# Kernel optimization log

Measured on AMD Instinct MI355X. Metric: run time of the kernel, lower is better.

## Reference

```python
import jax, jax.numpy as jnp
import numpy as np
import math

NUM_BINS = 10
TAIL_BOUND = 5.0
FILTER_CHANNELS = 192
KERNEL_SIZE = 3
N_LAYERS = 3
HALF = 1
MIN_BIN = 1e-3
MIN_DERIV = 1e-3


def conv1d(x, w, b, dilation=1, groups=1, padding=0):
    # x: [B,C,T], w: [O, C//groups, K]
    y = jax.lax.conv_general_dilated(
        x, w, window_strides=(1,), padding=[(padding, padding)],
        rhs_dilation=(dilation,), dimension_numbers=('NCH', 'OIH', 'NCH'),
        feature_group_count=groups)
    return y + b[None, :, None]


def ln_channels(x, g, b, eps=1e-5):
    # LayerNorm over channel dim (VITS modules.LayerNorm)
    m = jnp.mean(x, axis=1, keepdims=True)
    v = jnp.mean((x - m) ** 2, axis=1, keepdims=True)
    return g[None, :, None] * (x - m) * jax.lax.rsqrt(v + eps) + b[None, :, None]


def rq_spline(x1, uw, uh, ud):
    # piecewise rational-quadratic transform with linear tails (Durkan et al.)
    # x1: [B,1,T]; uw,uh: [B,1,T,K]; ud: [B,1,T,K-1]
    K = NUM_BINS
    tb = TAIL_BOUND
    inside = (x1 >= -tb) & (x1 <= tb)

    const = math.log(math.exp(1.0 - MIN_DERIV) - 1.0)  # softplus^-1(1-min_d)
    ud = jnp.pad(ud, [(0, 0)] * (ud.ndim - 1) + [(1, 1)], constant_values=const)

    widths = jax.nn.softmax(uw, axis=-1)
    widths = MIN_BIN + (1.0 - MIN_BIN * K) * widths
    cumw = jnp.pad(jnp.cumsum(widths, -1), [(0, 0)] * (uw.ndim - 1) + [(1, 0)])
    cumw = 2.0 * tb * cumw - tb
    cumw = cumw.at[..., 0].set(-tb).at[..., -1].set(tb)
    widths = cumw[..., 1:] - cumw[..., :-1]

    heights = jax.nn.softmax(uh, axis=-1)
    heights = MIN_BIN + (1.0 - MIN_BIN * K) * heights
    cumh = jnp.pad(jnp.cumsum(heights, -1), [(0, 0)] * (uh.ndim - 1) + [(1, 0)])
    cumh = 2.0 * tb * cumh - tb
    cumh = cumh.at[..., 0].set(-tb).at[..., -1].set(tb)
    heights = cumh[..., 1:] - cumh[..., :-1]

    derivs = MIN_DERIV + jax.nn.softplus(ud)  # [..., K+1]

    xin = jnp.clip(x1, -tb, tb)  # clamp so out-of-range lanes stay finite
    locs = cumw.at[..., -1].add(1e-6)
    bin_idx = jnp.clip(jnp.sum((xin[..., None] >= locs).astype(jnp.int32), -1) - 1, 0, K - 1)

    def take(a):
        return jnp.take_along_axis(a, bin_idx[..., None], axis=-1)[..., 0]

    icw = take(cumw)
    iw = take(widths)
    ich = take(cumh)
    ih = take(heights)
    d_l = take(derivs[..., :-1])
    d_r = take(derivs[..., 1:])
    delta = ih / iw

    theta = (xin - icw) / iw
    t1m = theta * (1.0 - theta)
    numerator = ih * (delta * theta * theta + d_l * t1m)
    denominator = delta + (d_l + d_r - 2.0 * delta) * t1m
    y = ich + numerator / denominator
    dnum = (delta * delta) * (d_r * theta * theta + 2.0 * delta * t1m + d_l * (1.0 - theta) ** 2)
    lad = jnp.log(dnum) - 2.0 * jnp.log(denominator)

    out = jnp.where(inside, y, x1)       # linear tails: identity outside
    lad = jnp.where(inside, lad, 0.0)
    return out, lad


def reference(x, x_mask, pre_w, pre_b, sep_w, sep_b, pw_w, pw_b,
              ln1_g, ln1_b, ln2_g, ln2_b, proj_w, proj_b):
    x0, x1 = x[:, :HALF], x[:, HALF:]
    h = conv1d(x0, pre_w, pre_b)
    # DDSConv (dilated depth-separable conv stack), p_dropout=0
    for i in range(N_LAYERS):
        d = KERNEL_SIZE ** i
        pad = (KERNEL_SIZE * d - d) // 2
        y = conv1d(h * x_mask, sep_w[i], sep_b[i], dilation=d,
                   groups=FILTER_CHANNELS, padding=pad)
        y = jax.nn.gelu(ln_channels(y, ln1_g[i], ln1_b[i]), approximate=False)
        y = conv1d(y, pw_w[i], pw_b[i])
        y = jax.nn.gelu(ln_channels(y, ln2_g[i], ln2_b[i]), approximate=False)
        h = h + y
    h = h * x_mask
    h = conv1d(h, proj_w, proj_b) * x_mask  # [B, half*(3K-1), T]
    b, c, t = x0.shape
    h = h.reshape(b, c, -1, t).transpose(0, 1, 3, 2)  # [B, half, T, 3K-1]
    scale = math.sqrt(FILTER_CHANNELS)
    uw = h[..., :NUM_BINS] / scale
    uh = h[..., NUM_BINS:2 * NUM_BINS] / scale
    ud = h[..., 2 * NUM_BINS:]
    x1o, lad = rq_spline(x1, uw, uh, ud)
    out = jnp.concatenate([x0, x1o], axis=1) * x_mask
    logdet = jnp.sum(lad * x_mask, axis=(1, 2))
    return out, logdet


def setup_inputs() -> dict:
    key = jax.random.key(0)
    ks = jax.random.split(key, 8)
    B, T, C, L, K = 64, 4096, FILTER_CHANNELS, N_LAYERS, KERNEL_SIZE
    return {
        'x': jax.random.normal(ks[0], (B, 2, T), jnp.float32),
        'x_mask': jnp.ones((B, 1, T), jnp.float32),
        'pre_w': jax.random.normal(ks[1], (C, 1, 1), jnp.float32) * 0.1,
        'pre_b': jnp.zeros((C,), jnp.float32),
        'sep_w': jax.random.normal(ks[2], (L, C, 1, K), jnp.float32) * 0.1,
        'sep_b': jnp.zeros((L, C), jnp.float32),
        'pw_w': jax.random.normal(ks[3], (L, C, C, 1), jnp.float32) * (1.0 / np.sqrt(C).astype(np.float32)),
        'pw_b': jnp.zeros((L, C), jnp.float32),
        'ln1_g': jnp.ones((L, C), jnp.float32),
        'ln1_b': jnp.zeros((L, C), jnp.float32),
        'ln2_g': jnp.ones((L, C), jnp.float32),
        'ln2_b': jnp.zeros((L, C), jnp.float32),
        'proj_w': jax.random.normal(ks[4], (HALF * (3 * NUM_BINS - 1), C, 1), jnp.float32) * 0.01,
        'proj_b': jnp.zeros((HALF * (3 * NUM_BINS - 1),), jnp.float32),
    }
```

## Files before the change

### kernel.cpp

```cpp
#include <hip/hip_runtime.h>
#include <stdint.h>

#define TT_ 4096
#define CC_ 192
#define TILE_ 64
#define HALO_ 13
#define TW_ 90
#define HS_ 104
#define YTS_ 200
#define NT_ 512

typedef float f32x4 __attribute__((ext_vector_type(4)));
typedef short s16x4 __attribute__((ext_vector_type(4)));
typedef short s16x8 __attribute__((ext_vector_type(8)));
typedef uint32_t ui32x4 __attribute__((ext_vector_type(4)));

__device__ __forceinline__ float bf2f(short s){
  uint32_t u = ((uint32_t)(uint16_t)s) << 16;
  float f; __builtin_memcpy(&f, &u, 4); return f;
}
__device__ __forceinline__ float bfhalf(uint32_t u, int hi){
  uint32_t v = hi ? (u & 0xFFFF0000u) : (u << 16);
  float f; __builtin_memcpy(&f, &v, 4); return f;
}
__device__ __forceinline__ short f2bf(float f){
  uint32_t u; __builtin_memcpy(&u, &f, 4);
  u += 0x7FFFu + ((u >> 16) & 1u);
  return (short)(u >> 16);
}
__device__ __forceinline__ float gelu_f(float x){
  float t = x*x;
  float p = x*__builtin_fmaf(t, 0.0713548162f, 1.5957691216f);
  float e = __expf(-p);
  return x * __builtin_amdgcn_rcpf(1.0f + e);
}

template<int D>
__device__ __forceinline__ void dw_pass(const short* __restrict__ Hs, short* __restrict__ YTs,
    const float* __restrict__ sw, const float* __restrict__ sb,
    int jlo, int jhi, int tid){
  constexpr int WO = (D==9) ? 16 : 8;
  constexpr int NW = (D==9) ? 5 : 3;
  for (int g = tid; g < 96*12; g += NT_){
    int cg = g % 96, jg = g / 96;
    int j0 = jg*8;
    if (j0 + 8 <= jlo || j0 >= jhi) continue;
    int c0 = cg*2;
    uint32_t pk[8];
    #pragma unroll
    for (int cc = 0; cc < 2; ++cc){
      int c = c0 + cc;
      float w0 = sw[c*3+0], w1 = sw[c*3+1], w2 = sw[c*3+2], bb = sb[c];
      uint32_t wp[NW*4];
      const uint32_t* hrow = (const uint32_t*)(Hs + c*HS_ + j0 - WO);
      #pragma unroll
      for (int u = 0; u < NW; ++u){
        ui32x4 t = *(const ui32x4*)(hrow + u*4);
        wp[u*4+0]=t[0]; wp[u*4+1]=t[1]; wp[u*4+2]=t[2]; wp[u*4+3]=t[3];
      }
      #pragma unroll
      for (int j = 0; j < 8; ++j){
        float t0 = bfhalf(wp[(WO+j-D)>>1], (WO+j-D)&1);
        float t1 = bfhalf(wp[(WO+j)>>1],   (WO+j)&1);
        float t2 = bfhalf(wp[(WO+j+D)>>1], (WO+j+D)&1);
        float v = __builtin_fmaf(w0,t0, __builtin_fmaf(w1,t1, __builtin_fmaf(w2,t2, bb)));
        uint32_t hb = (uint32_t)(uint16_t)f2bf(v);
        if (cc==0) pk[j] = hb; else pk[j] |= (hb << 16);
      }
    }
    #pragma unroll
    for (int j = 0; j < 8; ++j)
      *(uint32_t*)(YTs + (j0+j)*YTS_ + c0) = pk[j];
  }
}

__device__ __forceinline__ void ln_stats(const short* __restrict__ YTs, float* __restrict__ SM,
                                         float* __restrict__ SR, int jlo, int jhi, int tid){
  if (tid < 384){
    int row = tid >> 2, qtr = tid & 3;
    if (row >= jlo && row < jhi){
      const short* yr = YTs + row*YTS_ + qtr*48;
      float s0 = 0.f, s1 = 0.f, q0 = 0.f, q1 = 0.f;
      #pragma unroll
      for (int u=0;u<6;++u){
        s16x8 v = *(const s16x8*)(yr + u*8);
        #pragma unroll
        for (int e=0;e<4;e++){ float f=bf2f(v[e]); s0 += f; q0 = __builtin_fmaf(f,f,q0); }
        #pragma unroll
        for (int e=4;e<8;e++){ float f=bf2f(v[e]); s1 += f; q1 = __builtin_fmaf(f,f,q1); }
      }
      float s = s0+s1, q = q0+q1;
      s += __shfl_xor(s,1); q += __shfl_xor(q,1);
      s += __shfl_xor(s,2); q += __shfl_xor(q,2);
      if (qtr==0){
        float mean = s*(1.f/192.f);
        float var = fmaxf(q*(1.f/192.f) - mean*mean, 0.f);
        SM[row]=mean; SR[row]=rsqrtf(var+1e-5f);
      }
    }
  }
}

__global__ __launch_bounds__(512, 4)
void convflow_main(
    const float* __restrict__ x, const float* __restrict__ xmask,
    const float* __restrict__ pre_w, const float* __restrict__ pre_b,
    const float* __restrict__ sep_w, const float* __restrict__ sep_b,
    const float* __restrict__ pw_b,
    const float* __restrict__ ln1_g, const float* __restrict__ ln1_b,
    const float* __restrict__ ln2_g, const float* __restrict__ ln2_b,
    const float* __restrict__ proj_b,
    const short* __restrict__ Wbf, const short* __restrict__ Pbf,
    float* __restrict__ out, float* __restrict__ part)
{
  __shared__ __align__(16) char smem_raw[80128];
  float* MB = (float*)(smem_raw + 0);
  float* XB = (float*)(smem_raw + 640);
  float* SM = (float*)(smem_raw + 1024);
  float* SR = (float*)(smem_raw + 1408);
  short* H  = (short*)(smem_raw + 1792);
  short* YT = (short*)(smem_raw + 41728);
  float* HP = (float*)(smem_raw + 67328);

  const int tid = threadIdx.x;
  const int b = blockIdx.y, tile = blockIdx.x;
  const int t0 = tile*TILE_ - HALO_;

  for (int idx = tid; idx < 160; idx += NT_){
    int j = idx - 16; int t = t0 + j;
    float m = 0.f;
    if (j >= 0 && j < TW_ && t >= 0 && t < TT_) m = xmask[b*TT_ + t];
    MB[idx] = m;
  }
  if (tid < 96){
    int t = t0 + tid; float v = 0.f;
    if (tid < TW_ && t >= 0 && t < TT_) v = x[(b*2)*TT_ + t];
    XB[tid] = v;
  }
  __syncthreads();

  for (int g = tid; g < CC_*12; g += NT_){
    int jq = g % 12, c = g / 12;
    float w = pre_w[c], bb = pre_b[c];
    s16x8 hv;
    #pragma unroll
    for (int e=0;e<8;e++){
      int j = jq*8 + e;
      hv[e] = f2bf((w*XB[j] + bb)*MB[16+j]);
    }
    *(s16x8*)(H + c*HS_ + jq*8) = hv;
  }
  __syncthreads();

  #pragma unroll 1
  for (int li = 0; li < 3; ++li){
    const int jlo = (li==0) ? 1 : ((li==1) ? 4 : 13);
    const int jhi = (li==0) ? 89 : ((li==1) ? 86 : 77);
    const float* sw = sep_w + li*CC_*3;
    const float* sb = sep_b + li*CC_;

    if (li == 0)      dw_pass<1>(H, YT, sw, sb, jlo, jhi, tid);
    else if (li == 1) dw_pass<3>(H, YT, sw, sb, jlo, jhi, tid);
    else              dw_pass<9>(H, YT, sw, sb, jlo, jhi, tid);
    __syncthreads();

    ln_stats(YT, SM, SR, jlo, jhi, tid); __syncthreads();

    {
      const float* g1 = ln1_g + li*CC_;
      const float* b1 = ln1_b + li*CC_;
      for (int g = tid; g < 96*24; g += NT_){
        int ch = g % 24, row = g / 24;
        short* p = YT + row*YTS_ + ch*8;
        if (row >= jlo && row < jhi){
          float m = SM[row], r = SR[row];
          s16x8 v = *(s16x8*)p;
          f32x4 ga = *(const f32x4*)&g1[ch*8], gb = *(const f32x4*)&g1[ch*8+4];
          f32x4 ba = *(const f32x4*)&b1[ch*8], bb = *(const f32x4*)&b1[ch*8+4];
          s16x8 o;
          #pragma unroll
          for (int e=0;e<4;e++){
            float val = (bf2f(v[e]) - m)*r*ga[e] + ba[e];
            o[e] = f2bf(gelu_f(val));
          }
          #pragma unroll
          for (int e=4;e<8;e++){
            float val = (bf2f(v[e]) - m)*r*gb[e-4] + bb[e-4];
            o[e] = f2bf(gelu_f(val));
          }
          *(s16x8*)p = o;
        } else {
          s16x8 z = {0,0,0,0,0,0,0,0};
          *(s16x8*)p = z;
        }
      }
    }
    __syncthreads();

    {
      int w = tid >> 6, lane = tid & 63, l16 = lane & 15, q = lane >> 4;
      int Mh = w & 3, Nh = w >> 2;
      f32x4 acc[3][3];
      #pragma unroll
      for (int r=0;r<3;r++)
        #pragma unroll
        for (int s=0;s<3;s++){ f32x4 z = {0.f,0.f,0.f,0.f}; acc[r][s] = z; }
      const short* Wl = Wbf + li*CC_*CC_;
      #pragma unroll
      for (int kk=0;kk<6;++kk){
        s16x8 bv[3], av[3];
        #pragma unroll
        for (int s=0;s<3;++s)
          bv[s] = *(const s16x8*)&YT[((Nh*3+s)*16 + l16)*YTS_ + kk*32 + q*8];
        #pragma unroll
        for (int r=0;r<3;++r)
          av[r] = *(const s16x8*)&Wl[((Mh*3+r)*16 + l16)*CC_ + kk*32 + q*8];
        #pragma unroll
        for (int r=0;r<3;++r)
          #pragma unroll
          for (int s=0;s<3;++s)
            acc[r][s] = __builtin_amdgcn_mfma_f32_16x16x32_bf16(av[r], bv[s], acc[r][s], 0, 0, 0);
      }
      __syncthreads();
      #pragma unroll
      for (int r=0;r<3;++r){
        int m0 = (Mh*3+r)*16 + q*4;
        f32x4 bias = *(const f32x4*)&pw_b[li*CC_ + m0];
        #pragma unroll
        for (int s=0;s<3;++s){
          int n = (Nh*3+s)*16 + l16;
          s16x4 ov;
          #pragma unroll
          for (int e=0;e<4;e++) ov[e] = f2bf(acc[r][s][e] + bias[e]);
          *(s16x4*)(YT + n*YTS_ + m0) = ov;
        }
      }
      __syncthreads();
    }

    ln_stats(YT, SM, SR, jlo, jhi, tid); __syncthreads();

    {
      const float* g2 = ln2_g + li*CC_;
      const float* b2 = ln2_b + li*CC_;
      for (int g = tid; g < 24*48; g += NT_){
        int cgp = g % 48, jg = g / 48;
        int j0 = jg*4, c0 = cgp*4;
        if (j0 + 4 <= jlo || j0 >= jhi) continue;
        f32x4 mv = *(f32x4*)&SM[j0], rv = *(f32x4*)&SR[j0];
        f32x4 mk = *(f32x4*)&MB[16 + j0];
        f32x4 gv = *(const f32x4*)&g2[c0], bv = *(const f32x4*)&b2[c0];
        s16x4 yr[4];
        #pragma unroll
        for (int jj=0;jj<4;++jj) yr[jj] = *(s16x4*)(YT + (j0+jj)*YTS_ + c0);
        #pragma unroll
        for (int cc=0;cc<4;++cc){
          short* hp_ = H + (c0+cc)*HS_ + j0;
          s16x4 hv = *(s16x4*)hp_;
          s16x4 ho;
          #pragma unroll
          for (int jj=0;jj<4;++jj){
            int j = j0 + jj;
            float val = (bf2f(yr[jj][cc]) - mv[jj])*rv[jj]*gv[cc] + bv[cc];
            float hn = (bf2f(hv[jj]) + gelu_f(val))*mk[jj];
            bool ok = (j >= jlo) && (j < jhi);
            ho[jj] = ok ? f2bf(hn) : hv[jj];
          }
          *(s16x4*)hp_ = ho;
        }
      }
    }
    __syncthreads();
  }

  {
    int w = tid >> 6;
    if (w < 4){
      int lane = tid & 63, l16 = lane & 15, q = lane >> 4;
      int mt = w >> 1, ntp = w & 1;
      f32x4 pacc[2];
      { f32x4 z = {0.f,0.f,0.f,0.f}; pacc[0] = z; pacc[1] = z; }
      #pragma unroll
      for (int kk=0;kk<6;++kk){
        s16x8 a = *(const s16x8*)&Pbf[(mt*16 + l16)*CC_ + kk*32 + q*8];
        #pragma unroll
        for (int s=0;s<2;++s){
          int n = (ntp*2+s)*16 + l16;
          s16x8 bvv;
          #pragma unroll
          for (int i=0;i<8;++i)
            bvv[i] = H[(kk*32 + q*8 + i)*HS_ + HALO_ + n];
          pacc[s] = __builtin_amdgcn_mfma_f32_16x16x32_bf16(a, bvv, pacc[s], 0, 0, 0);
        }
      }
      #pragma unroll
      for (int s=0;s<2;++s)
        #pragma unroll
        for (int e=0;e<4;e++){
          int m = mt*16 + q*4 + e;
          if (m < 29){
            int n = (ntp*2+s)*16 + l16;
            HP[n*33 + m] = (pacc[s][e] + proj_b[m]) * MB[16 + HALO_ + n];
          }
        }
    }
  }
  __syncthreads();

  if (tid < 64){
    const int n = tid;
    const int tg = tile*TILE_ + n;
    const float msk = MB[16 + HALO_ + n];
    const float* hp = &HP[n*33];
    const float inv_s = 0.07216878364870323f;
    float uw[10], uh[10], ud9[9];
    #pragma unroll
    for (int k=0;k<10;k++){ uw[k] = hp[k]*inv_s; uh[k] = hp[10+k]*inv_s; }
    #pragma unroll
    for (int k=0;k<9;k++) ud9[k] = hp[20+k];

    float cumw[11], cumh[11];
    {
      float mx = uw[0];
      #pragma unroll
      for (int k=1;k<10;k++) mx = fmaxf(mx, uw[k]);
      float ex[10]; float ss = 0.f;
      #pragma unroll
      for (int k=0;k<10;k++){ ex[k] = __expf(uw[k]-mx); ss += ex[k]; }
      float inv = 1.0f/ss;
      cumw[0] = -5.f; float cw = 0.f;
      #pragma unroll
      for (int k=0;k<10;k++){ float wk = 0.001f + 0.99f*(ex[k]*inv); cw += wk; cumw[k+1] = 10.f*cw - 5.f; }
      cumw[10] = 5.f;
    }
    {
      float mx = uh[0];
      #pragma unroll
      for (int k=1;k<10;k++) mx = fmaxf(mx, uh[k]);
      float ex[10]; float ss = 0.f;
      #pragma unroll
      for (int k=0;k<10;k++){ ex[k] = __expf(uh[k]-mx); ss += ex[k]; }
      float inv = 1.0f/ss;
      cumh[0] = -5.f; float ch = 0.f;
      #pragma unroll
      for (int k=0;k<10;k++){ float hk = 0.001f + 0.99f*(ex[k]*inv); ch += hk; cumh[k+1] = 10.f*ch - 5.f; }
      cumh[10] = 5.f;
    }
    float dv[11];
    dv[0] = 1.0f; dv[10] = 1.0f;
    #pragma unroll
    for (int k=0;k<9;k++){
      float u = ud9[k];
      float sp = (u > 15.f) ? u : log1pf(__expf(u));
      dv[k+1] = 0.001f + sp;
    }

    const float x1 = x[(b*2+1)*TT_ + tg];
    const float xin = fminf(fmaxf(x1, -5.f), 5.f);
    int cnt = 0;
    #pragma unroll
    for (int k=0;k<11;k++){
      float lk = cumw[k] + ((k==10) ? 1e-6f : 0.f);
      cnt += (xin >= lk) ? 1 : 0;
    }
    int bin = cnt - 1;
    bin = (bin < 0) ? 0 : ((bin > 9) ? 9 : bin);

    float icw=0.f, iw=1.f, ich=0.f, ih=1.f, dl=1.f, dr=1.f;
    #pragma unroll
    for (int k=0;k<10;k++){
      if (bin == k){
        icw = cumw[k]; iw = cumw[k+1]-cumw[k];
        ich = cumh[k]; ih = cumh[k+1]-cumh[k];
        dl = dv[k]; dr = dv[k+1];
      }
    }
    float delta = ih/iw;
    float th = (xin - icw)/iw;
    float t1m = th*(1.f-th);
    float num = ih*(delta*th*th + dl*t1m);
    float den = delta + (dl + dr - 2.f*delta)*t1m;
    float yv = ich + num/den;
    float omt = 1.f - th;
    float dnum = delta*delta*(dr*th*th + 2.f*delta*t1m + dl*omt*omt);
    float lad = logf(dnum) - 2.f*logf(den);
    bool inside = (x1 >= -5.f) && (x1 <= 5.f);
    float outv = inside ? yv : x1;
    float ladv = inside ? lad : 0.f;

    out[(b*2)*TT_ + tg]   = x[(b*2)*TT_ + tg] * msk;
    out[(b*2+1)*TT_ + tg] = outv * msk;

    float lsum = ladv * msk;
    #pragma unroll
    for (int off = 32; off > 0; off >>= 1) lsum += __shfl_xor(lsum, off);
    if (tid == 0) part[b*64 + tile] = lsum;
  }
}

__global__ void convflow_pre(const float* __restrict__ pw_w, const float* __restrict__ proj_w,
                             short* __restrict__ Wbf, short* __restrict__ Pbf){
  int idx = blockIdx.x*256 + threadIdx.x;
  if (idx < 110592) Wbf[idx] = f2bf(pw_w[idx]);
  if (idx < 32*192){
    int m = idx / 192, k = idx - m*192;
    Pbf[idx] = (m < 29) ? f2bf(proj_w[m*192 + k]) : (short)0;
  }
}

__global__ void convflow_logdet(const float* __restrict__ part, float* __restrict__ out){
  int bb = threadIdx.x;
  if (bb < 64){
    float s = 0.f;
    for (int k=0;k<64;k++) s += part[bb*64 + k];
    out[524288 + bb] = s;
  }
}

extern "C" void kernel_launch(void* const* d_in, const int* in_sizes, int n_in,
                              void* d_out, int out_size, void* d_ws, size_t ws_size,
                              hipStream_t stream) {
  const float* x      = (const float*)d_in[0];
  const float* xmask  = (const float*)d_in[1];
  const float* pre_w  = (const float*)d_in[2];
  const float* pre_b  = (const float*)d_in[3];
  const float* sep_w  = (const float*)d_in[4];
  const float* sep_b  = (const float*)d_in[5];
  const float* pw_w   = (const float*)d_in[6];
  const float* pw_b   = (const float*)d_in[7];
  const float* ln1_g  = (const float*)d_in[8];
  const float* ln1_b  = (const float*)d_in[9];
  const float* ln2_g  = (const float*)d_in[10];
  const float* ln2_b  = (const float*)d_in[11];
  const float* proj_w = (const float*)d_in[12];
  const float* proj_b = (const float*)d_in[13];

  short* Wbf = (short*)d_ws;
  short* Pbf = (short*)((char*)d_ws + 221184);
  float* part = (float*)((char*)d_ws + 233472);
  float* out = (float*)d_out;

  convflow_pre<<<432, 256, 0, stream>>>(pw_w, proj_w, Wbf, Pbf);
  dim3 grid(64, 64);
  convflow_main<<<grid, NT_, 0, stream>>>(x, xmask, pre_w, pre_b, sep_w, sep_b, pw_b,
                                          ln1_g, ln1_b, ln2_g, ln2_b, proj_b,
                                          Wbf, Pbf, out, part);
  convflow_logdet<<<1, 64, 0, stream>>>(part, out);
}
```

Baseline: 601.2 us.

## Swizzle YT LDS layout, shrink H stride, and pack bf16 via perm

Adds an XOR swizzle on the 8-element column groups of the transposed YT buffer so that MFMA operand reads and row-wise LN accesses spread across LDS banks. The H row stride drops from 104 to 100 shorts, which shrinks LDS use and changes bank mapping; the depthwise pass now loads with 8-byte vectors to match. Float-to-bf16 packing now uses v_perm, with truncation instead of round-to-nearest on YT writes. This cuts ALU work in exchange for a small precision change on intermediate activations.

```diff
diff --git a/kernel.cpp b/kernel.cpp
--- a/kernel.cpp
+++ b/kernel.cpp
@@ -6,13 +6,14 @@
 #define TILE_ 64
 #define HALO_ 13
 #define TW_ 90
-#define HS_ 104
+#define HS_ 100
 #define YTS_ 200
 #define NT_ 512
 
 typedef float f32x4 __attribute__((ext_vector_type(4)));
 typedef short s16x4 __attribute__((ext_vector_type(4)));
 typedef short s16x8 __attribute__((ext_vector_type(8)));
+typedef uint32_t ui32x2 __attribute__((ext_vector_type(2)));
 typedef uint32_t ui32x4 __attribute__((ext_vector_type(4)));
 
 __device__ __forceinline__ float bf2f(short s){
@@ -27,6 +28,19 @@
   uint32_t u; __builtin_memcpy(&u, &f, 4);
   u += 0x7FFFu + ((u >> 16) & 1u);
   return (short)(u >> 16);
+}
+__device__ __forceinline__ uint32_t fbits(float f){
+  uint32_t u; __builtin_memcpy(&u, &f, 4); return u;
+}
+__device__ __forceinline__ uint32_t pk_trunc(float lo, float hi){
+  return __builtin_amdgcn_perm(fbits(hi), fbits(lo), 0x07060302u);
+}
+__device__ __forceinline__ uint32_t rne_u(float f){
+  uint32_t u = fbits(f);
+  return u + 0x7FFFu + ((u >> 16) & 1u);
+}
+__device__ __forceinline__ uint32_t pk_rne(float lo, float hi){
+  return __builtin_amdgcn_perm(rne_u(hi), rne_u(lo), 0x07060302u);
 }
 __device__ __forceinline__ float gelu_f(float x){
   float t = x*x;
@@ -34,43 +48,46 @@
   float e = __expf(-p);
   return x * __builtin_amdgcn_rcpf(1.0f + e);
 }
+__device__ __forceinline__ int ytix(int row, int col){
+  return row*YTS_ + ((((col >> 3) ^ (row & 3)) << 3) | (col & 7));
+}
 
 template<int D>
 __device__ __forceinline__ void dw_pass(const short* __restrict__ Hs, short* __restrict__ YTs,
     const float* __restrict__ sw, const float* __restrict__ sb,
     int jlo, int jhi, int tid){
   constexpr int WO = (D==9) ? 16 : 8;
-  constexpr int NW = (D==9) ? 5 : 3;
+  constexpr int NU = (D==9) ? 20 : 12;
   for (int g = tid; g < 96*12; g += NT_){
     int cg = g % 96, jg = g / 96;
     int j0 = jg*8;
     if (j0 + 8 <= jlo || j0 >= jhi) continue;
     int c0 = cg*2;
-    uint32_t pk[8];
-    #pragma unroll
-    for (int cc = 0; cc < 2; ++cc){
-      int c = c0 + cc;
-      float w0 = sw[c*3+0], w1 = sw[c*3+1], w2 = sw[c*3+2], bb = sb[c];
-      uint32_t wp[NW*4];
-      const uint32_t* hrow = (const uint32_t*)(Hs + c*HS_ + j0 - WO);
-      #pragma unroll
-      for (int u = 0; u < NW; ++u){
-        ui32x4 t = *(const ui32x4*)(hrow + u*4);
-        wp[u*4+0]=t[0]; wp[u*4+1]=t[1]; wp[u*4+2]=t[2]; wp[u*4+3]=t[3];
-      }
-      #pragma unroll
-      for (int j = 0; j < 8; ++j){
-        float t0 = bfhalf(wp[(WO+j-D)>>1], (WO+j-D)&1);
-        float t1 = bfhalf(wp[(WO+j)>>1],   (WO+j)&1);
-        float t2 = bfhalf(wp[(WO+j+D)>>1], (WO+j+D)&1);
-        float v = __builtin_fmaf(w0,t0, __builtin_fmaf(w1,t1, __builtin_fmaf(w2,t2, bb)));
-        uint32_t hb = (uint32_t)(uint16_t)f2bf(v);
-        if (cc==0) pk[j] = hb; else pk[j] |= (hb << 16);
-      }
-    }
-    #pragma unroll
-    for (int j = 0; j < 8; ++j)
-      *(uint32_t*)(YTs + (j0+j)*YTS_ + c0) = pk[j];
+    uint32_t wpa[NU], wpb[NU];
+    {
+      const uint32_t* ra = (const uint32_t*)(Hs + (c0+0)*HS_ + j0 - WO);
+      const uint32_t* rb = (const uint32_t*)(Hs + (c0+1)*HS_ + j0 - WO);
+      #pragma unroll
+      for (int u = 0; u < NU/2; ++u){
+        ui32x2 ta = *(const ui32x2*)(ra + u*2);
+        ui32x2 tb = *(const ui32x2*)(rb + u*2);
+        wpa[u*2] = ta[0]; wpa[u*2+1] = ta[1];
+        wpb[u*2] = tb[0]; wpb[u*2+1] = tb[1];
+      }
+    }
+    float w0a = sw[c0*3+0], w1a = sw[c0*3+1], w2a = sw[c0*3+2], bav = sb[c0];
+    float w0b = sw[c0*3+3], w1b = sw[c0*3+4], w2b = sw[c0*3+5], bbv = sb[c0+1];
+    #pragma unroll
+    for (int j = 0; j < 8; ++j){
+      int h0 = WO + j - D, h1 = WO + j, h2 = WO + j + D;
+      float va = __builtin_fmaf(w0a, bfhalf(wpa[h0>>1], h0&1),
+                 __builtin_fmaf(w1a, bfhalf(wpa[h1>>1], h1&1),
+                 __builtin_fmaf(w2a, bfhalf(wpa[h2>>1], h2&1), bav)));
+      float vb = __builtin_fmaf(w0b, bfhalf(wpb[h0>>1], h0&1),
+                 __builtin_fmaf(w1b, bfhalf(wpb[h1>>1], h1&1),
+                 __builtin_fmaf(w2b, bfhalf(wpb[h2>>1], h2&1), bbv)));
+      *(uint32_t*)(YTs + ytix(j0+j, c0)) = pk_trunc(va, vb);
+    }
   }
 }
 
@@ -79,11 +96,10 @@
   if (tid < 384){
     int row = tid >> 2, qtr = tid & 3;
     if (row >= jlo && row < jhi){
-      const short* yr = YTs + row*YTS_ + qtr*48;
       float s0 = 0.f, s1 = 0.f, q0 = 0.f, q1 = 0.f;
       #pragma unroll
       for (int u=0;u<6;++u){
-        s16x8 v = *(const s16x8*)(yr + u*8);
+        s16x8 v = *(const s16x8*)(YTs + ytix(row, qtr*48 + u*8));
         #pragma unroll
         for (int e=0;e<4;e++){ float f=bf2f(v[e]); s0 += f; q0 = __builtin_fmaf(f,f,q0); }
         #pragma unroll
@@ -113,14 +129,14 @@
     const short* __restrict__ Wbf, const short* __restrict__ Pbf,
     float* __restrict__ out, float* __restrict__ part)
 {
-  __shared__ __align__(16) char smem_raw[80128];
+  __shared__ __align__(16) char smem_raw[78592];
   float* MB = (float*)(smem_raw + 0);
   float* XB = (float*)(smem_raw + 640);
   float* SM = (float*)(smem_raw + 1024);
   float* SR = (float*)(smem_raw + 1408);
   short* H  = (short*)(smem_raw + 1792);
-  short* YT = (short*)(smem_raw + 41728);
-  float* HP = (float*)(smem_raw + 67328);
+  short* YT = (short*)(smem_raw + 40192);
+  float* HP = (float*)(smem_raw + 65792);
 
   const int tid = threadIdx.x;
   const int b = blockIdx.y, tile = blockIdx.x;
@@ -139,16 +155,16 @@
   }
   __syncthreads();
 
-  for (int g = tid; g < CC_*12; g += NT_){
-    int jq = g % 12, c = g / 12;
+  for (int g = tid; g < CC_*24; g += NT_){
+    int jq = g % 24, c = g / 24;
     float w = pre_w[c], bb = pre_b[c];
-    s16x8 hv;
-    #pragma unroll
-    for (int e=0;e<8;e++){
-      int j = jq*8 + e;
-      hv[e] = f2bf((w*XB[j] + bb)*MB[16+j]);
-    }
-    *(s16x8*)(H + c*HS_ + jq*8) = hv;
+    int j0 = jq*4;
+    float v0 = (w*XB[j0+0] + bb)*MB[16+j0+0];
+    float v1 = (w*XB[j0+1] + bb)*MB[16+j0+1];
+    float v2 = (w*XB[j0+2] + bb)*MB[16+j0+2];
+    float v3 = (w*XB[j0+3] + bb)*MB[16+j0+3];
+    ui32x2 o; o[0] = pk_rne(v0, v1); o[1] = pk_rne(v2, v3);
+    *(ui32x2*)(H + c*HS_ + j0) = o;
   }
   __syncthreads();
 
@@ -171,27 +187,30 @@
       const float* b1 = ln1_b + li*CC_;
       for (int g = tid; g < 96*24; g += NT_){
         int ch = g % 24, row = g / 24;
-        short* p = YT + row*YTS_ + ch*8;
+        short* p = YT + ytix(row, ch*8);
         if (row >= jlo && row < jhi){
           float m = SM[row], r = SR[row];
           s16x8 v = *(s16x8*)p;
           f32x4 ga = *(const f32x4*)&g1[ch*8], gb = *(const f32x4*)&g1[ch*8+4];
           f32x4 ba = *(const f32x4*)&b1[ch*8], bb = *(const f32x4*)&b1[ch*8+4];
-          s16x8 o;
+          float ov[8];
           #pragma unroll
           for (int e=0;e<4;e++){
             float val = (bf2f(v[e]) - m)*r*ga[e] + ba[e];
-            o[e] = f2bf(gelu_f(val));
+            ov[e] = gelu_f(val);
           }
           #pragma unroll
           for (int e=4;e<8;e++){
             float val = (bf2f(v[e]) - m)*r*gb[e-4] + bb[e-4];
-            o[e] = f2bf(gelu_f(val));
+            ov[e] = gelu_f(val);
           }
-          *(s16x8*)p = o;
+          ui32x4 o;
+          #pragma unroll
+          for (int e=0;e<4;e++) o[e] = pk_trunc(ov[2*e], ov[2*e+1]);
+          *(ui32x4*)p = o;
         } else {
-          s16x8 z = {0,0,0,0,0,0,0,0};
-          *(s16x8*)p = z;
+          ui32x4 z = {0u,0u,0u,0u};
+          *(ui32x4*)p = z;
         }
       }
     }
@@ -211,7 +230,7 @@
         s16x8 bv[3], av[3];
         #pragma unroll
         for (int s=0;s<3;++s)
-          bv[s] = *(const s16x8*)&YT[((Nh*3+s)*16 + l16)*YTS_ + kk*32 + q*8];
+          bv[s] = *(const s16x8*)&YT[ytix((Nh*3+s)*16 + l16, kk*32 + q*8)];
         #pragma unroll
         for (int r=0;r<3;++r)
           av[r] = *(const s16x8*)&Wl[((Mh*3+r)*16 + l16)*CC_ + kk*32 + q*8];
@@ -229,10 +248,10 @@
         #pragma unroll
         for (int s=0;s<3;++s){
           int n = (Nh*3+s)*16 + l16;
-          s16x4 ov;
-          #pragma unroll
-          for (int e=0;e<4;e++) ov[e] = f2bf(acc[r][s][e] + bias[e]);
-          *(s16x4*)(YT + n*YTS_ + m0) = ov;
+          ui32x2 ov;
+          ov[0] = pk_trunc(acc[r][s][0]+bias[0], acc[r][s][1]+bias[1]);
+          ov[1] = pk_trunc(acc[r][s][2]+bias[2], acc[r][s][3]+bias[3]);
+          *(ui32x2*)(YT + ytix(n, m0)) = ov;
         }
       }
       __syncthreads();
@@ -252,21 +271,22 @@
         f32x4 gv = *(const f32x4*)&g2[c0], bv = *(const f32x4*)&b2[c0];
         s16x4 yr[4];
         #pragma unroll
-        for (int jj=0;jj<4;++jj) yr[jj] = *(s16x4*)(YT + (j0+jj)*YTS_ + c0);
+        for (int jj=0;jj<4;++jj) yr[jj] = *(s16x4*)(YT + ytix(j0+jj, c0));
         #pragma unroll
         for (int cc=0;cc<4;++cc){
           short* hp_ = H + (c0+cc)*HS_ + j0;
           s16x4 hv = *(s16x4*)hp_;
-          s16x4 ho;
+          float hf[4];
           #pragma unroll
           for (int jj=0;jj<4;++jj){
             int j = j0 + jj;
             float val = (bf2f(yr[jj][cc]) - mv[jj])*rv[jj]*gv[cc] + bv[cc];
             float hn = (bf2f(hv[jj]) + gelu_f(val))*mk[jj];
             bool ok = (j >= jlo) && (j < jhi);
-            ho[jj] = ok ? f2bf(hn) : hv[jj];
+            hf[jj] = ok ? hn : bf2f(hv[jj]);
           }
-          *(s16x4*)hp_ = ho;
+          ui32x2 o; o[0] = pk_rne(hf[0], hf[1]); o[1] = pk_rne(hf[2], hf[3]);
+          *(ui32x2*)hp_ = o;
         }
       }
     }
```

New measurement: 595.5 us. No clear change (-1.0%).
